# Performance work log

Measured on AMD Instinct MI355X. Metric: run time of the kernel, lower is better.

Reference implementation:

```python
import jax, jax.numpy as jnp
import numpy as np

B, L, D, H = 1, 2048, 1024, 16
DH = D // H            # head dim = 64
RD = 16                # rope dim = dim_head / 4 (partial RoPE)
SCALE = DH ** -0.5
NEG = -1e9


def _layernorm(x, g, b, eps=1e-5):
    m = jnp.mean(x, -1, keepdims=True)
    v = jnp.mean((x - m) ** 2, -1, keepdims=True)
    return (x - m) * jax.lax.rsqrt(v + eps) * g + b


def _rope_tables(length, rd):
    # GPT-NeoX style: freqs over rd/2, duplicated via concat
    inv_freq = 1.0 / (10000.0 ** (jnp.arange(0, rd, 2, dtype=jnp.float32) / rd))
    t = jnp.arange(length, dtype=jnp.float32)
    f = t[:, None] * inv_freq[None, :]          # [L, rd/2]
    f = jnp.concatenate([f, f], -1)             # [L, rd]
    return jnp.cos(f)[None, None], jnp.sin(f)[None, None]  # [1,1,L,rd]


def _apply_rope(x, cos, sin):
    # rotate only the first RD dims of each head; pass the rest through
    rd = cos.shape[-1]
    xr, xp = x[..., :rd], x[..., rd:]
    x1, x2 = jnp.split(xr, 2, axis=-1)
    rot = jnp.concatenate([-x2, x1], -1)
    return jnp.concatenate([xr * cos + rot * sin, xp], -1)


def _alibi_causal_bias(length, num_heads):
    # per-head ALiBi slope + causal mask (AttentionBiasMask: ['alibi','causal'])
    slopes = 2.0 ** (-8.0 * (jnp.arange(num_heads, dtype=jnp.float32) + 1) / num_heads)
    i = jnp.arange(length)
    rel = i[:, None] - i[None, :]               # [L, L], >=0 on/below diagonal
    bias = -slopes[:, None, None] * rel[None].astype(jnp.float32)
    bias = jnp.where(rel[None] >= 0, bias, NEG)  # causal mask
    return bias[None]                            # [1, H, L, L]


def setup_inputs() -> dict:
    key = jax.random.key(0)
    ks = jax.random.split(key, 8)
    s = 0.02
    return {
        "x": jax.random.normal(ks[0], (B, L, D), jnp.float32),
        "previous_attn_dots": jax.random.normal(ks[1], (B, H, L, L), jnp.float32) * 0.1,
        "Wq": jax.random.normal(ks[2], (D, D), jnp.float32) * s,
        "Wk": jax.random.normal(ks[3], (D, D), jnp.float32) * s,
        "Wv": jax.random.normal(ks[4], (D, D), jnp.float32) * s,
        "Wo": jax.random.normal(ks[5], (D, D), jnp.float32) * s,
        "bo": jnp.zeros((D,), jnp.float32),
        "gamma": jnp.ones((D,), jnp.float32),
        "beta": jnp.zeros((D,), jnp.float32),
        "Wg": jax.random.normal(ks[6], (D, D), jnp.float32) * s,
        "bg": jnp.zeros((D,), jnp.float32),
    }


def reference(x, previous_attn_dots, Wq, Wk, Wv, Wo, bo, gamma, beta, Wg, bg):
    residual = x
    cos, sin = _rope_tables(L, RD)
    bias = _alibi_causal_bias(L, H)

    h = _layernorm(x, gamma, beta)

    def heads(t):  # [B,L,D] -> [B,H,L,DH]
        return t.reshape(B, L, H, DH).transpose(0, 2, 1, 3)

    q = _apply_rope(heads(h @ Wq), cos, sin)
    k = _apply_rope(heads(h @ Wk), cos, sin)
    v = _apply_rope(heads(h @ Wv), cos, sin)  # rotate_v_bool=True

    dots = jnp.einsum('bhid,bhjd->bhij', q, k) * SCALE
    dots = dots + previous_attn_dots          # residual attention
    dots = dots + bias                        # ALiBi + causal
    attn_map = jax.nn.softmax(dots, axis=-1)

    o = jnp.einsum('bhij,bhjd->bhid', attn_map, v)
    o = o.transpose(0, 2, 1, 3).reshape(B, L, D)
    y = o @ Wo + bo

    gate = jax.nn.sigmoid(residual @ Wg + bg)  # output_gate ('sigmoid','on_residual')
    y = gate * y
    y = y + residual                           # add_residual
    return (y, attn_map, dots)
```

## Files before the change

### kernel.cpp

```cpp
#include <hip/hip_runtime.h>
#include <hip/hip_bf16.h>
#include <math.h>

#define LLEN 2048
#define DMODEL 1024
#define NHEAD 16
#define DHEAD 64
#define SCALE 0.125f
#define NEGF -1000000000.0f

typedef __attribute__((ext_vector_type(8))) short short8;
typedef __attribute__((ext_vector_type(4))) float f32x4;

__device__ __forceinline__ unsigned short f2bf(float f) {
  union { float f; unsigned u; } cv; cv.f = f;
  unsigned u = cv.u;
  u += 0x7FFF + ((u >> 16) & 1);
  return (unsigned short)(u >> 16);
}

__global__ __launch_bounds__(256) void transpose_w(
    const float* __restrict__ Wq, const float* __restrict__ Wk,
    const float* __restrict__ Wv, const float* __restrict__ Wo,
    const float* __restrict__ Wg,
    unsigned short* __restrict__ Wqt, unsigned short* __restrict__ Wkt,
    unsigned short* __restrict__ Wvt, unsigned short* __restrict__ Wot,
    unsigned short* __restrict__ Wgt) {
  const float* W; unsigned short* Wt;
  switch (blockIdx.z) {
    case 0: W = Wq; Wt = Wqt; break;
    case 1: W = Wk; Wt = Wkt; break;
    case 2: W = Wv; Wt = Wvt; break;
    case 3: W = Wo; Wt = Wot; break;
    default: W = Wg; Wt = Wgt; break;
  }
  __shared__ unsigned short tile[64][72];
  int k0 = blockIdx.y * 64, n0 = blockIdx.x * 64;
  int c4 = (threadIdx.x & 15) * 4, r = threadIdx.x >> 4;
  for (int rr = r; rr < 64; rr += 16) {
    float4 v = *(const float4*)(W + (size_t)(k0 + rr) * DMODEL + n0 + c4);
    tile[rr][c4 + 0] = f2bf(v.x); tile[rr][c4 + 1] = f2bf(v.y);
    tile[rr][c4 + 2] = f2bf(v.z); tile[rr][c4 + 3] = f2bf(v.w);
  }
  __syncthreads();
  for (int rr = r; rr < 64; rr += 16) {
    ushort4 o;
    o.x = tile[c4 + 0][rr]; o.y = tile[c4 + 1][rr];
    o.z = tile[c4 + 2][rr]; o.w = tile[c4 + 3][rr];
    *(ushort4*)(Wt + (size_t)(n0 + rr) * DMODEL + k0 + c4) = o;
  }
}

__global__ __launch_bounds__(256) void ln_kernel(
    const float* __restrict__ x, const float* __restrict__ gamma,
    const float* __restrict__ beta,
    unsigned short* __restrict__ hb, unsigned short* __restrict__ xb) {
  int l = blockIdx.x, t = threadIdx.x;
  float4 v = ((const float4*)(x + (size_t)l * DMODEL))[t];
  float s  = v.x + v.y + v.z + v.w;
  float s2 = v.x * v.x + v.y * v.y + v.z * v.z + v.w * v.w;
  for (int off = 32; off; off >>= 1) {
    s  += __shfl_down(s, off);
    s2 += __shfl_down(s2, off);
  }
  __shared__ float rs[4], rs2[4];
  int wave = t >> 6, lane = t & 63;
  if (lane == 0) { rs[wave] = s; rs2[wave] = s2; }
  __syncthreads();
  float mean = (rs[0] + rs[1] + rs[2] + rs[3]) * (1.0f / DMODEL);
  float var  = (rs2[0] + rs2[1] + rs2[2] + rs2[3]) * (1.0f / DMODEL) - mean * mean;
  float rstd = rsqrtf(var + 1e-5f);
  float4 g = ((const float4*)gamma)[t];
  float4 b = ((const float4*)beta)[t];
  ushort4 hh, xx;
  hh.x = f2bf((v.x - mean) * rstd * g.x + b.x);
  hh.y = f2bf((v.y - mean) * rstd * g.y + b.y);
  hh.z = f2bf((v.z - mean) * rstd * g.z + b.z);
  hh.w = f2bf((v.w - mean) * rstd * g.w + b.w);
  xx.x = f2bf(v.x); xx.y = f2bf(v.y); xx.z = f2bf(v.z); xx.w = f2bf(v.w);
  ((ushort4*)(hb + (size_t)l * DMODEL))[t] = hh;
  ((ushort4*)(xb + (size_t)l * DMODEL))[t] = xx;
}

__device__ __forceinline__ void mfma_gemm_64x64(
    const unsigned short* __restrict__ A, const unsigned short* __restrict__ Bt,
    int row0, int ncol0, int lm, int quad, f32x4 acc[4]) {
  for (int k0 = 0; k0 < DMODEL; k0 += 64) {
    short8 a0 = *(const short8*)(A + (size_t)(row0 + lm) * DMODEL + k0 + quad * 8);
    short8 a1 = *(const short8*)(A + (size_t)(row0 + lm) * DMODEL + k0 + 32 + quad * 8);
#pragma unroll
    for (int c = 0; c < 4; c++) {
      const unsigned short* bp = Bt + (size_t)(ncol0 + c * 16 + lm) * DMODEL + k0 + quad * 8;
      short8 b0 = *(const short8*)(bp);
      short8 b1 = *(const short8*)(bp + 32);
      acc[c] = __builtin_amdgcn_mfma_f32_16x16x32_bf16(a0, b0, acc[c], 0, 0, 0);
      acc[c] = __builtin_amdgcn_mfma_f32_16x16x32_bf16(a1, b1, acc[c], 0, 0, 0);
    }
  }
}

__global__ __launch_bounds__(256) void gemm_qkv(
    const unsigned short* __restrict__ hb,
    const unsigned short* __restrict__ Wqt, const unsigned short* __restrict__ Wkt,
    const unsigned short* __restrict__ Wvt,
    unsigned short* __restrict__ qb, unsigned short* __restrict__ kb,
    unsigned short* __restrict__ vT) {
  int which = blockIdx.z;
  const unsigned short* Bt = (which == 0) ? Wqt : (which == 1) ? Wkt : Wvt;
  int wave = threadIdx.x >> 6, lane = threadIdx.x & 63;
  int lm = lane & 15, quad = lane >> 4;
  int it = blockIdx.x, head = blockIdx.y;
  int row0 = it * 64 + wave * 16;
  f32x4 acc[4] = {};
  mfma_gemm_64x64(hb, Bt, row0, head * 64, lm, quad, acc);
  __shared__ float tile[64][65];
#pragma unroll
  for (int c = 0; c < 4; c++)
#pragma unroll
    for (int r2 = 0; r2 < 4; r2++)
      tile[wave * 16 + quad * 4 + r2][c * 16 + lm] = acc[c][r2];
  __syncthreads();
  int r = threadIdx.x >> 2, seg = threadIdx.x & 3;
  int lrow = it * 64 + r;
  float vals[16];
#pragma unroll
  for (int i2 = 0; i2 < 16; i2++) vals[i2] = tile[r][seg * 16 + i2];
  if (seg == 0) {
    float outv[16];
#pragma unroll
    for (int j = 0; j < 8; j++) {
      float invf = powf(10000.f, -(float)j * 0.125f);
      float f = (float)lrow * invf;
      float cs = cosf(f), sn = sinf(f);
      outv[j]     = vals[j] * cs - vals[j + 8] * sn;
      outv[j + 8] = vals[j + 8] * cs + vals[j] * sn;
    }
#pragma unroll
    for (int j = 0; j < 16; j++) vals[j] = outv[j];
  }
  if (which < 2) {
    unsigned short* dst = ((which == 0) ? qb : kb) + ((size_t)head * LLEN + lrow) * DHEAD + seg * 16;
    union { unsigned short u[16]; uint4 v[2]; } tmp;
#pragma unroll
    for (int i2 = 0; i2 < 16; i2++) tmp.u[i2] = f2bf(vals[i2]);
    *(uint4*)dst = tmp.v[0];
    *((uint4*)dst + 1) = tmp.v[1];
  } else {
    __syncthreads();
#pragma unroll
    for (int i2 = 0; i2 < 16; i2++) tile[r][seg * 16 + i2] = vals[i2];
    __syncthreads();
    int dh = threadIdx.x >> 2, ls = threadIdx.x & 3;
    union { unsigned short u[16]; uint4 v[2]; } tmp;
#pragma unroll
    for (int i2 = 0; i2 < 16; i2++) tmp.u[i2] = f2bf(tile[ls * 16 + i2][dh]);
    unsigned short* dst = vT + ((size_t)head * DHEAD + dh) * LLEN + it * 64 + ls * 16;
    *(uint4*)dst = tmp.v[0];
    *((uint4*)dst + 1) = tmp.v[1];
  }
}

__global__ __launch_bounds__(128) void attn_kernel(
    const unsigned short* __restrict__ qb, const unsigned short* __restrict__ kb,
    const unsigned short* __restrict__ vT, const float* __restrict__ prev,
    float* __restrict__ dots, float* __restrict__ attn,
    unsigned short* __restrict__ ob) {
  int it2 = blockIdx.x, h = blockIdx.y;
  int wave = threadIdx.x >> 6, lane = threadIdx.x & 63;
  int lm = lane & 15, quad = lane >> 4;
  int row0 = it2 * 32 + wave * 16;
  const unsigned short* q = qb + (size_t)h * LLEN * DHEAD;
  const unsigned short* k = kb + (size_t)h * LLEN * DHEAD;
  const unsigned short* v = vT + (size_t)h * DHEAD * LLEN;
  const float* pr = prev + (size_t)h * LLEN * LLEN;
  float* drow = dots + (size_t)h * LLEN * LLEN;
  float* arow = attn + (size_t)h * LLEN * LLEN;
  short8 qa0 = *(const short8*)(q + (size_t)(row0 + lm) * DHEAD + quad * 8);
  short8 qa1 = *(const short8*)(q + (size_t)(row0 + lm) * DHEAD + 32 + quad * 8);
  float slope = exp2f(-8.0f * (float)(h + 1) / (float)NHEAD);
  float m[4] = {-1e30f, -1e30f, -1e30f, -1e30f};
  float lsum[4] = {0.f, 0.f, 0.f, 0.f};
  int jt_max = it2 >> 1;
  for (int jt = 0; jt <= jt_max; jt++) {
    f32x4 s[4];
#pragma unroll
    for (int c = 0; c < 4; c++) {
      const unsigned short* kp = k + (size_t)(jt * 64 + c * 16 + lm) * DHEAD + quad * 8;
      short8 b0 = *(const short8*)kp;
      short8 b1 = *(const short8*)(kp + 32);
      f32x4 z = {};
      z = __builtin_amdgcn_mfma_f32_16x16x32_bf16(qa0, b0, z, 0, 0, 0);
      z = __builtin_amdgcn_mfma_f32_16x16x32_bf16(qa1, b1, z, 0, 0, 0);
      s[c] = z;
    }
#pragma unroll
    for (int c = 0; c < 4; c++) {
      int j = jt * 64 + c * 16 + lm;
#pragma unroll
      for (int r = 0; r < 4; r++) {
        int i = row0 + quad * 4 + r;
        float pv = pr[(size_t)i * LLEN + j];
        float bias = (i >= j) ? (-slope * (float)(i - j)) : NEGF;
        float d = s[c][r] * SCALE + pv + bias;
        drow[(size_t)i * LLEN + j] = d;
        s[c][r] = d;
      }
    }
#pragma unroll
    for (int r = 0; r < 4; r++) {
      float mx = fmaxf(fmaxf(s[0][r], s[1][r]), fmaxf(s[2][r], s[3][r]));
#pragma unroll
      for (int off = 1; off < 16; off <<= 1)
        mx = fmaxf(mx, __shfl_xor(mx, off, 16));
      float mnew = fmaxf(m[r], mx);
      float sum = __expf(s[0][r] - mnew) + __expf(s[1][r] - mnew) +
                  __expf(s[2][r] - mnew) + __expf(s[3][r] - mnew);
#pragma unroll
      for (int off = 1; off < 16; off <<= 1)
        sum += __shfl_xor(sum, off, 16);
      lsum[r] = lsum[r] * __expf(m[r] - mnew) + sum;
      m[r] = mnew;
    }
  }
  f32x4 oacc[4] = {};
  __shared__ __align__(16) unsigned short pt[2][16][72];
  float rinv[4];
#pragma unroll
  for (int r = 0; r < 4; r++) rinv[r] = 1.0f / lsum[r];
  for (int jt = 0; jt <= jt_max; jt++) {
#pragma unroll
    for (int c = 0; c < 4; c++) {
      int j = jt * 64 + c * 16 + lm;
#pragma unroll
      for (int r = 0; r < 4; r++) {
        int i = row0 + quad * 4 + r;
        float d = drow[(size_t)i * LLEN + j];
        float p = __expf(d - m[r]) * rinv[r];
        arow[(size_t)i * LLEN + j] = p;
        pt[wave][quad * 4 + r][c * 16 + lm] = f2bf(p);
      }
    }
    __syncthreads();
    short8 pa0 = *(const short8*)&pt[wave][lm][quad * 8];
    short8 pa1 = *(const short8*)&pt[wave][lm][32 + quad * 8];
#pragma unroll
    for (int c = 0; c < 4; c++) {
      const unsigned short* vp = v + (size_t)(c * 16 + lm) * LLEN + jt * 64 + quad * 8;
      short8 b0 = *(const short8*)vp;
      short8 b1 = *(const short8*)(vp + 32);
      oacc[c] = __builtin_amdgcn_mfma_f32_16x16x32_bf16(pa0, b0, oacc[c], 0, 0, 0);
      oacc[c] = __builtin_amdgcn_mfma_f32_16x16x32_bf16(pa1, b1, oacc[c], 0, 0, 0);
    }
    __syncthreads();
  }
#pragma unroll
  for (int c = 0; c < 4; c++)
#pragma unroll
    for (int r = 0; r < 4; r++)
      ob[(size_t)(row0 + quad * 4 + r) * DMODEL + h * DHEAD + c * 16 + lm] = f2bf(oacc[c][r]);
  int jstart = (jt_max + 1) * 64;
  int ncols4 = (LLEN - jstart) >> 2;
  if (ncols4 > 0) {
    float4 negv = {NEGF, NEGF, NEGF, NEGF};
    float4 zero = {0.f, 0.f, 0.f, 0.f};
    int r = threadIdx.x >> 2, t4 = threadIdx.x & 3;
    size_t base = (size_t)(it2 * 32 + r) * LLEN + jstart;
    for (int c4 = t4; c4 < ncols4; c4 += 4) {
      *(float4*)(drow + base + c4 * 4) = negv;
      *(float4*)(arow + base + c4 * 4) = zero;
    }
  }
}

__global__ __launch_bounds__(256) void gemm_gate(
    const unsigned short* __restrict__ xb, const unsigned short* __restrict__ Wgt,
    const float* __restrict__ bg, float* __restrict__ gate) {
  int wave = threadIdx.x >> 6, lane = threadIdx.x & 63;
  int lm = lane & 15, quad = lane >> 4;
  int row0 = blockIdx.x * 64 + wave * 16, ncol0 = blockIdx.y * 64;
  f32x4 acc[4] = {};
  mfma_gemm_64x64(xb, Wgt, row0, ncol0, lm, quad, acc);
#pragma unroll
  for (int c = 0; c < 4; c++) {
    int col = ncol0 + c * 16 + lm;
    float bgv = bg[col];
#pragma unroll
    for (int r = 0; r < 4; r++) {
      int i = row0 + quad * 4 + r;
      float g = acc[c][r] + bgv;
      gate[(size_t)i * DMODEL + col] = 1.0f / (1.0f + __expf(-g));
    }
  }
}

__global__ __launch_bounds__(256) void gemm_out(
    const unsigned short* __restrict__ ob, const unsigned short* __restrict__ Wot,
    const float* __restrict__ bo, const float* __restrict__ gate,
    const float* __restrict__ x, float* __restrict__ y) {
  int wave = threadIdx.x >> 6, lane = threadIdx.x & 63;
  int lm = lane & 15, quad = lane >> 4;
  int row0 = blockIdx.x * 64 + wave * 16, ncol0 = blockIdx.y * 64;
  f32x4 acc[4] = {};
  mfma_gemm_64x64(ob, Wot, row0, ncol0, lm, quad, acc);
#pragma unroll
  for (int c = 0; c < 4; c++) {
    int col = ncol0 + c * 16 + lm;
    float bov = bo[col];
#pragma unroll
    for (int r = 0; r < 4; r++) {
      int i = row0 + quad * 4 + r;
      size_t idx = (size_t)i * DMODEL + col;
      float y0 = acc[c][r] + bov;
      y[idx] = gate[idx] * y0 + x[idx];
    }
  }
}

extern "C" void kernel_launch(void* const* d_in, const int* in_sizes, int n_in,
                              void* d_out, int out_size, void* d_ws, size_t ws_size,
                              hipStream_t stream) {
  const float* x     = (const float*)d_in[0];
  const float* prev  = (const float*)d_in[1];
  const float* Wq    = (const float*)d_in[2];
  const float* Wk    = (const float*)d_in[3];
  const float* Wv    = (const float*)d_in[4];
  const float* Wo    = (const float*)d_in[5];
  const float* bo    = (const float*)d_in[6];
  const float* gamma = (const float*)d_in[7];
  const float* beta  = (const float*)d_in[8];
  const float* Wg    = (const float*)d_in[9];
  const float* bg    = (const float*)d_in[10];

  float* y    = (float*)d_out;
  float* attn = y + 2097152;
  float* dots = attn + 67108864;

  char* ws = (char*)d_ws;
  unsigned short* hb  = (unsigned short*)(ws + 0);
  unsigned short* xb  = (unsigned short*)(ws + 4194304);
  unsigned short* Wqt = (unsigned short*)(ws + 8388608);
  unsigned short* Wkt = (unsigned short*)(ws + 10485760);
  unsigned short* Wvt = (unsigned short*)(ws + 12582912);
  unsigned short* Wot = (unsigned short*)(ws + 14680064);
  unsigned short* Wgt = (unsigned short*)(ws + 16777216);
  unsigned short* qb  = (unsigned short*)(ws + 18874368);
  unsigned short* kb  = (unsigned short*)(ws + 23068672);
  unsigned short* vT  = (unsigned short*)(ws + 27262976);
  unsigned short* ob  = (unsigned short*)(ws + 31457280);
  float*          gate = (float*)(ws + 35651584);

  transpose_w<<<dim3(16, 16, 5), 256, 0, stream>>>(Wq, Wk, Wv, Wo, Wg, Wqt, Wkt, Wvt, Wot, Wgt);
  ln_kernel<<<dim3(2048), 256, 0, stream>>>(x, gamma, beta, hb, xb);
  gemm_qkv<<<dim3(32, 16, 3), 256, 0, stream>>>(hb, Wqt, Wkt, Wvt, qb, kb, vT);
  attn_kernel<<<dim3(64, 16), 128, 0, stream>>>(qb, kb, vT, prev, dots, attn, ob);
  gemm_gate<<<dim3(32, 16), 256, 0, stream>>>(xb, Wgt, bg, gate);
  gemm_out<<<dim3(32, 16), 256, 0, stream>>>(ob, Wot, bo, gate, x, y);
}
```

Baseline: 1.137 ms.

## Drop online max, fuse PV into the score pass, normalise attn in a separate kernel

The attention kernel now computes exp(d) without subtracting a running row max. It accumulates the row sums and the unnormalised P·V in a single pass over the keys, then scales the output by the inverse sum and stores that inverse per row. A new attn_norm kernel rereads dots and writes the normalised attention map, including the zero region. Each block now handles a short query tile and a long one (g and 127-g) to balance the causal work, and the block-wide barriers around the per-wave LDS tile are removed. Skipping the max subtraction means exp can overflow if logits exceed about 88, so correctness depends on the logits staying within that range.

```diff
diff --git a/kernel.cpp b/kernel.cpp
--- a/kernel.cpp
+++ b/kernel.cpp
@@ -163,111 +163,125 @@
 __global__ __launch_bounds__(128) void attn_kernel(
     const unsigned short* __restrict__ qb, const unsigned short* __restrict__ kb,
     const unsigned short* __restrict__ vT, const float* __restrict__ prev,
-    float* __restrict__ dots, float* __restrict__ attn,
-    unsigned short* __restrict__ ob) {
-  int it2 = blockIdx.x, h = blockIdx.y;
-  int wave = threadIdx.x >> 6, lane = threadIdx.x & 63;
+    float* __restrict__ dots, unsigned short* __restrict__ ob,
+    float* __restrict__ rinvg) {
+  int h = blockIdx.y;
+  int wv = threadIdx.x >> 6, lane = threadIdx.x & 63;
   int lm = lane & 15, quad = lane >> 4;
-  int row0 = it2 * 32 + wave * 16;
+  int g0 = blockIdx.x * 2 + wv;
   const unsigned short* q = qb + (size_t)h * LLEN * DHEAD;
   const unsigned short* k = kb + (size_t)h * LLEN * DHEAD;
   const unsigned short* v = vT + (size_t)h * DHEAD * LLEN;
   const float* pr = prev + (size_t)h * LLEN * LLEN;
   float* drow = dots + (size_t)h * LLEN * LLEN;
-  float* arow = attn + (size_t)h * LLEN * LLEN;
-  short8 qa0 = *(const short8*)(q + (size_t)(row0 + lm) * DHEAD + quad * 8);
-  short8 qa1 = *(const short8*)(q + (size_t)(row0 + lm) * DHEAD + 32 + quad * 8);
   float slope = exp2f(-8.0f * (float)(h + 1) / (float)NHEAD);
-  float m[4] = {-1e30f, -1e30f, -1e30f, -1e30f};
-  float lsum[4] = {0.f, 0.f, 0.f, 0.f};
-  int jt_max = it2 >> 1;
-  for (int jt = 0; jt <= jt_max; jt++) {
-    f32x4 s[4];
-#pragma unroll
-    for (int c = 0; c < 4; c++) {
-      const unsigned short* kp = k + (size_t)(jt * 64 + c * 16 + lm) * DHEAD + quad * 8;
-      short8 b0 = *(const short8*)kp;
-      short8 b1 = *(const short8*)(kp + 32);
-      f32x4 z = {};
-      z = __builtin_amdgcn_mfma_f32_16x16x32_bf16(qa0, b0, z, 0, 0, 0);
-      z = __builtin_amdgcn_mfma_f32_16x16x32_bf16(qa1, b1, z, 0, 0, 0);
-      s[c] = z;
-    }
-#pragma unroll
-    for (int c = 0; c < 4; c++) {
-      int j = jt * 64 + c * 16 + lm;
-#pragma unroll
-      for (int r = 0; r < 4; r++) {
-        int i = row0 + quad * 4 + r;
-        float pv = pr[(size_t)i * LLEN + j];
-        float bias = (i >= j) ? (-slope * (float)(i - j)) : NEGF;
-        float d = s[c][r] * SCALE + pv + bias;
-        drow[(size_t)i * LLEN + j] = d;
-        s[c][r] = d;
+  __shared__ __align__(16) unsigned short pt[2][16][72];
+
+  for (int pass = 0; pass < 2; ++pass) {
+    int g = pass ? (127 - g0) : g0;
+    int row0 = g * 16;
+    int jt_end = g >> 2;
+    short8 qa0 = *(const short8*)(q + (size_t)(row0 + lm) * DHEAD + quad * 8);
+    short8 qa1 = *(const short8*)(q + (size_t)(row0 + lm) * DHEAD + 32 + quad * 8);
+    f32x4 oacc[4] = {};
+    float lsum[4] = {0.f, 0.f, 0.f, 0.f};
+    for (int jt = 0; jt <= jt_end; jt++) {
+      f32x4 s[4];
+#pragma unroll
+      for (int c = 0; c < 4; c++) {
+        const unsigned short* kp = k + (size_t)(jt * 64 + c * 16 + lm) * DHEAD + quad * 8;
+        short8 b0 = *(const short8*)kp;
+        short8 b1 = *(const short8*)(kp + 32);
+        f32x4 z = {};
+        z = __builtin_amdgcn_mfma_f32_16x16x32_bf16(qa0, b0, z, 0, 0, 0);
+        z = __builtin_amdgcn_mfma_f32_16x16x32_bf16(qa1, b1, z, 0, 0, 0);
+        s[c] = z;
       }
-    }
+#pragma unroll
+      for (int c = 0; c < 4; c++) {
+        int j = jt * 64 + c * 16 + lm;
+#pragma unroll
+        for (int r = 0; r < 4; r++) {
+          int i = row0 + quad * 4 + r;
+          int rel = i - j;
+          float bias = (rel >= 0) ? (-slope * (float)rel) : NEGF;
+          float d = fmaf(s[c][r], SCALE, pr[(size_t)i * LLEN + j]) + bias;
+          drow[(size_t)i * LLEN + j] = d;
+          float p = __expf(d);
+          lsum[r] += p;
+          pt[wv][quad * 4 + r][c * 16 + lm] = f2bf(p);
+        }
+      }
+      short8 pa0 = *(const short8*)&pt[wv][lm][quad * 8];
+      short8 pa1 = *(const short8*)&pt[wv][lm][32 + quad * 8];
+#pragma unroll
+      for (int c = 0; c < 4; c++) {
+        const unsigned short* vp = v + (size_t)(c * 16 + lm) * LLEN + jt * 64 + quad * 8;
+        short8 b0 = *(const short8*)vp;
+        short8 b1 = *(const short8*)(vp + 32);
+        oacc[c] = __builtin_amdgcn_mfma_f32_16x16x32_bf16(pa0, b0, oacc[c], 0, 0, 0);
+        oacc[c] = __builtin_amdgcn_mfma_f32_16x16x32_bf16(pa1, b1, oacc[c], 0, 0, 0);
+      }
+    }
+    float rv[4];
 #pragma unroll
     for (int r = 0; r < 4; r++) {
-      float mx = fmaxf(fmaxf(s[0][r], s[1][r]), fmaxf(s[2][r], s[3][r]));
-#pragma unroll
-      for (int off = 1; off < 16; off <<= 1)
-        mx = fmaxf(mx, __shfl_xor(mx, off, 16));
-      float mnew = fmaxf(m[r], mx);
-      float sum = __expf(s[0][r] - mnew) + __expf(s[1][r] - mnew) +
-                  __expf(s[2][r] - mnew) + __expf(s[3][r] - mnew);
-#pragma unroll
-      for (int off = 1; off < 16; off <<= 1)
-        sum += __shfl_xor(sum, off, 16);
-      lsum[r] = lsum[r] * __expf(m[r] - mnew) + sum;
-      m[r] = mnew;
-    }
-  }
-  f32x4 oacc[4] = {};
-  __shared__ __align__(16) unsigned short pt[2][16][72];
-  float rinv[4];
-#pragma unroll
-  for (int r = 0; r < 4; r++) rinv[r] = 1.0f / lsum[r];
-  for (int jt = 0; jt <= jt_max; jt++) {
-#pragma unroll
-    for (int c = 0; c < 4; c++) {
-      int j = jt * 64 + c * 16 + lm;
-#pragma unroll
-      for (int r = 0; r < 4; r++) {
-        int i = row0 + quad * 4 + r;
-        float d = drow[(size_t)i * LLEN + j];
-        float p = __expf(d - m[r]) * rinv[r];
-        arow[(size_t)i * LLEN + j] = p;
-        pt[wave][quad * 4 + r][c * 16 + lm] = f2bf(p);
+      float sm = lsum[r];
+#pragma unroll
+      for (int off = 1; off < 16; off <<= 1) sm += __shfl_xor(sm, off, 16);
+      rv[r] = 1.0f / sm;
+    }
+#pragma unroll
+    for (int c = 0; c < 4; c++)
+#pragma unroll
+      for (int r = 0; r < 4; r++)
+        ob[(size_t)(row0 + quad * 4 + r) * DMODEL + h * DHEAD + c * 16 + lm] =
+            f2bf(oacc[c][r] * rv[r]);
+    if (lm == 0) {
+#pragma unroll
+      for (int r = 0; r < 4; r++)
+        rinvg[(size_t)h * LLEN + row0 + quad * 4 + r] = rv[r];
+    }
+    int jstart = (jt_end + 1) * 64;
+    int ncols4 = (LLEN - jstart) >> 2;
+    if (ncols4 > 0) {
+      float4 negv = {NEGF, NEGF, NEGF, NEGF};
+      int r = lane >> 2, t4 = lane & 3;
+      size_t base = (size_t)(row0 + r) * LLEN + jstart;
+      for (int c4 = t4; c4 < ncols4; c4 += 4)
+        *(float4*)(drow + base + c4 * 4) = negv;
+    }
+  }
+}
+
+__global__ __launch_bounds__(256) void attn_norm(
+    const float* __restrict__ dots, const float* __restrict__ rinvg,
+    float* __restrict__ attn) {
+  int h = blockIdx.y;
+  int i0 = blockIdx.x * 8;
+  const float* dr = dots + (size_t)h * LLEN * LLEN;
+  float* ar = attn + (size_t)h * LLEN * LLEN;
+#pragma unroll
+  for (int rr = 0; rr < 8; rr++) {
+    int i = i0 + rr;
+    float rinv = rinvg[(size_t)h * LLEN + i];
+    int nwr4 = ((i >> 6) + 1) * 16;
+#pragma unroll
+    for (int jc = 0; jc < 2; jc++) {
+      int j4 = threadIdx.x + jc * 256;
+      size_t idx = (size_t)i * LLEN + (size_t)j4 * 4;
+      if (j4 < nwr4) {
+        float4 d = *(const float4*)(dr + idx);
+        float4 o;
+        o.x = __expf(d.x) * rinv;
+        o.y = __expf(d.y) * rinv;
+        o.z = __expf(d.z) * rinv;
+        o.w = __expf(d.w) * rinv;
+        *(float4*)(ar + idx) = o;
+      } else {
+        float4 z = {0.f, 0.f, 0.f, 0.f};
+        *(float4*)(ar + idx) = z;
       }
-    }
-    __syncthreads();
-    short8 pa0 = *(const short8*)&pt[wave][lm][quad * 8];
-    short8 pa1 = *(const short8*)&pt[wave][lm][32 + quad * 8];
-#pragma unroll
-    for (int c = 0; c < 4; c++) {
-      const unsigned short* vp = v + (size_t)(c * 16 + lm) * LLEN + jt * 64 + quad * 8;
-      short8 b0 = *(const short8*)vp;
-      short8 b1 = *(const short8*)(vp + 32);
-      oacc[c] = __builtin_amdgcn_mfma_f32_16x16x32_bf16(pa0, b0, oacc[c], 0, 0, 0);
-      oacc[c] = __builtin_amdgcn_mfma_f32_16x16x32_bf16(pa1, b1, oacc[c], 0, 0, 0);
-    }
-    __syncthreads();
-  }
-#pragma unroll
-  for (int c = 0; c < 4; c++)
-#pragma unroll
-    for (int r = 0; r < 4; r++)
-      ob[(size_t)(row0 + quad * 4 + r) * DMODEL + h * DHEAD + c * 16 + lm] = f2bf(oacc[c][r]);
-  int jstart = (jt_max + 1) * 64;
-  int ncols4 = (LLEN - jstart) >> 2;
-  if (ncols4 > 0) {
-    float4 negv = {NEGF, NEGF, NEGF, NEGF};
-    float4 zero = {0.f, 0.f, 0.f, 0.f};
-    int r = threadIdx.x >> 2, t4 = threadIdx.x & 3;
-    size_t base = (size_t)(it2 * 32 + r) * LLEN + jstart;
-    for (int c4 = t4; c4 < ncols4; c4 += 4) {
-      *(float4*)(drow + base + c4 * 4) = negv;
-      *(float4*)(arow + base + c4 * 4) = zero;
     }
   }
 }
@@ -348,11 +362,13 @@
   unsigned short* vT  = (unsigned short*)(ws + 27262976);
   unsigned short* ob  = (unsigned short*)(ws + 31457280);
   float*          gate = (float*)(ws + 35651584);
+  float*          rinvg = (float*)(ws + 0);
 
   transpose_w<<<dim3(16, 16, 5), 256, 0, stream>>>(Wq, Wk, Wv, Wo, Wg, Wqt, Wkt, Wvt, Wot, Wgt);
   ln_kernel<<<dim3(2048), 256, 0, stream>>>(x, gamma, beta, hb, xb);
   gemm_qkv<<<dim3(32, 16, 3), 256, 0, stream>>>(hb, Wqt, Wkt, Wvt, qb, kb, vT);
-  attn_kernel<<<dim3(64, 16), 128, 0, stream>>>(qb, kb, vT, prev, dots, attn, ob);
+  attn_kernel<<<dim3(32, 16), 128, 0, stream>>>(qb, kb, vT, prev, dots, ob, rinvg);
+  attn_norm<<<dim3(256, 16), 256, 0, stream>>>(dots, rinvg, attn);
   gemm_gate<<<dim3(32, 16), 256, 0, stream>>>(xb, Wgt, bg, gate);
   gemm_out<<<dim3(32, 16), 256, 0, stream>>>(ob, Wot, bo, gate, x, y);
 }
```

Measured after the change: 1.216 ms. 7.0% more time.
